# Optimization experiments

Hardware: AMD Instinct MI355X
Metric: run time of the kernel (lower is better)

The kernel has to match this reference:

```python
import jax, jax.numpy as jnp
import numpy as np

MASK_NUM = -2.0 ** 32 + 1.0  # additive mask value from the module


def setup_inputs() -> dict:
    key = jax.random.key(0)
    k1, k2, k3, k4 = jax.random.split(key, 4)
    BH, S, D = 32, 2048, 64   # batch*heads, seq, head_dim
    B = 2                      # true batch for key padding masks
    q = jax.random.normal(k1, (BH, S, D), dtype=jnp.float32)
    k = jax.random.normal(k2, (BH, S, D), dtype=jnp.float32)
    v = jax.random.normal(k3, (BH, S, D), dtype=jnp.float32)
    masks = jax.random.randint(k4, (B, S), 0, 2, dtype=jnp.int32)  # 1 = masked key
    return {"q": q, "k": k, "v": v, "masks": masks}


def reference(q, k, v, masks):
    # scores: [BH, Sq, Sk]
    d = q.shape[-1]
    scores = jnp.einsum("bqd,bkd->bqk", q, k) / jnp.sqrt(jnp.float32(d))
    # tile key-padding masks over heads: [B,Sk] -> [BH,Sk], add big negative
    tile = q.shape[0] // masks.shape[0]
    m = jnp.tile(masks.astype(jnp.float32), (tile, 1))  # [BH, Sk]
    scores = scores + m[:, None, :] * MASK_NUM
    attn = jax.nn.softmax(scores, axis=-1)
    # dropout rate is 0.0 -> identity
    out = jnp.einsum("bqk,bkd->bqd", attn, v)
    return out
```

## Files before the change

kernel.cpp:

```cpp
#include <hip/hip_runtime.h>
#include <hip/hip_bf16.h>


#define SQ 2048
#define DD 64
#define NT 32

typedef __attribute__((ext_vector_type(8)))  short bf16x8;
typedef __attribute__((ext_vector_type(16))) float f32x16;

#define LOG2E  1.4426950408889634f
#define QSCALE (0.125f * LOG2E)
#define MASKV  (-4294967295.0f * LOG2E)
#define THRL   (8.0f * LOG2E)

__device__ __forceinline__ short f2bf(float x) {
    union { float f; unsigned u; } a; a.f = x;
    unsigned r = a.u + 0x7fffu + ((a.u >> 16) & 1u);
    return (short)(r >> 16);
}
__device__ __forceinline__ int cvt_pk(float lo, float hi) {
    int r;
    asm("v_cvt_pk_bf16_f32 %0, %1, %2" : "=v"(r) : "v"(lo), "v"(hi));
    return r;
}
__device__ __forceinline__ int swz(int row, int colByte) {
    return row * 128 + (colByte ^ ((row & 7) << 4));
}

__global__ __launch_bounds__(256, 2) void attn_fwd(
    const float* __restrict__ q, const float* __restrict__ k,
    const float* __restrict__ v, const int* __restrict__ masks,
    float* __restrict__ out)
{
    __shared__ alignas(16) char smem[24576];
    char*  Kb = smem;
    char*  Vb = smem + 8192;
    float* Mf = (float*)(smem + 16384);

    const int x    = blockIdx.x;
    const int orig = (x & 7) * 64 + (x >> 3);
    const int h    = orig >> 4;
    const int qb   = orig & 15;
    const int tid  = threadIdx.x;
    const int w    = tid >> 6;
    const int lane = tid & 63;
    const int l31  = lane & 31;
    const int hi   = lane >> 5;

    const float* __restrict__ qh = q + (size_t)h * SQ * DD;
    const float* __restrict__ kh = k + (size_t)h * SQ * DD;
    const float* __restrict__ vh = v + (size_t)h * SQ * DD;
    const int*   __restrict__ mrow = masks + (h & 1) * SQ;

    {
        int4 a = *(const int4*)(mrow + tid * 8);
        int4 b = *(const int4*)(mrow + tid * 8 + 4);
        float4 fa = { a.x ? MASKV : 0.f, a.y ? MASKV : 0.f,
                      a.z ? MASKV : 0.f, a.w ? MASKV : 0.f };
        float4 fb = { b.x ? MASKV : 0.f, b.y ? MASKV : 0.f,
                      b.z ? MASKV : 0.f, b.w ? MASKV : 0.f };
        *(float4*)(Mf + tid * 8)     = fa;
        *(float4*)(Mf + tid * 8 + 4) = fb;
    }

    const int qrow = qb * 128 + w * 32 + l31;
    bf16x8 qf[4];
#pragma unroll
    for (int dc = 0; dc < 4; ++dc) {
        const float* p = qh + (size_t)qrow * DD + dc * 16 + hi * 8;
        float4 a = *(const float4*)p;
        float4 b = *(const float4*)(p + 4);
        bf16x8 f;
        f[0] = f2bf(a.x * QSCALE); f[1] = f2bf(a.y * QSCALE);
        f[2] = f2bf(a.z * QSCALE); f[3] = f2bf(a.w * QSCALE);
        f[4] = f2bf(b.x * QSCALE); f[5] = f2bf(b.y * QSCALE);
        f[6] = f2bf(b.z * QSCALE); f[7] = f2bf(b.w * QSCALE);
        qf[dc] = f;
    }

    f32x16 o[2];
#pragma unroll
    for (int dt = 0; dt < 2; ++dt)
#pragma unroll
      for (int i = 0; i < 16; ++i) o[dt][i] = 0.f;
    float m = -3.0e38f, l = 0.f;

    const int rK = tid >> 3, cK = tid & 7;
    const int kV = tid & 63, dV = (tid >> 6) * 8;

    float4 kA0, kA1, kB0, kB1, vA0, vA1, vB0, vB1;
#define LOADKV(kt)                                                        \
    {   const float* kpA = kh + (size_t)((kt) + rK)      * DD + 8 * cK;  \
        const float* kpB = kh + (size_t)((kt) + rK + 32) * DD + 8 * cK;  \
        const float* vpA = vh + (size_t)((kt) + kV) * DD + dV;           \
        const float* vpB = vpA + 32;                                      \
        kA0 = *(const float4*)kpA; kA1 = *(const float4*)(kpA + 4);      \
        kB0 = *(const float4*)kpB; kB1 = *(const float4*)(kpB + 4);      \
        vA0 = *(const float4*)vpA; vA1 = *(const float4*)(vpA + 4);      \
        vB0 = *(const float4*)vpB; vB1 = *(const float4*)(vpB + 4);      }

#define WRITEKV()                                                         \
    {   bf16x8 kw;                                                        \
        kw[0]=f2bf(kA0.x); kw[1]=f2bf(kA0.y); kw[2]=f2bf(kA0.z); kw[3]=f2bf(kA0.w); \
        kw[4]=f2bf(kA1.x); kw[5]=f2bf(kA1.y); kw[6]=f2bf(kA1.z); kw[7]=f2bf(kA1.w); \
        *(bf16x8*)(Kb + swz(rK, 16 * cK)) = kw;                           \
        kw[0]=f2bf(kB0.x); kw[1]=f2bf(kB0.y); kw[2]=f2bf(kB0.z); kw[3]=f2bf(kB0.w); \
        kw[4]=f2bf(kB1.x); kw[5]=f2bf(kB1.y); kw[6]=f2bf(kB1.z); kw[7]=f2bf(kB1.w); \
        *(bf16x8*)(Kb + swz(rK + 32, 16 * cK)) = kw;                      \
        float va[8] = {vA0.x, vA0.y, vA0.z, vA0.w, vA1.x, vA1.y, vA1.z, vA1.w}; \
        float vb[8] = {vB0.x, vB0.y, vB0.z, vB0.w, vB1.x, vB1.y, vB1.z, vB1.w}; \
        _Pragma("unroll")                                                 \
        for (int j = 0; j < 8; ++j) {                                     \
            *(short*)(Vb + (dV + j)      * 128 + ((2 * kV) ^ (j << 4))) = f2bf(va[j]); \
            *(short*)(Vb + (dV + 32 + j) * 128 + ((2 * kV) ^ (j << 4))) = f2bf(vb[j]); \
        }                                                                 }

    LOADKV(0)
    WRITEKV()
    __syncthreads();

    for (int it = 0; it < NT; ++it) {
        const int kt = it * 64;
        if (it + 1 < NT) LOADKV(kt + 64)

        const float* mf = Mf + kt;
        f32x16 s0, s1;
#pragma unroll
        for (int g = 0; g < 4; ++g) {
            float4 m0 = *(const float4*)(mf + 8 * g + 4 * hi);
            float4 m1 = *(const float4*)(mf + 32 + 8 * g + 4 * hi);
            s0[4*g+0] = m0.x; s0[4*g+1] = m0.y; s0[4*g+2] = m0.z; s0[4*g+3] = m0.w;
            s1[4*g+0] = m1.x; s1[4*g+1] = m1.y; s1[4*g+2] = m1.z; s1[4*g+3] = m1.w;
        }
#pragma unroll
        for (int dc = 0; dc < 4; ++dc) {
            bf16x8 k0 = *(const bf16x8*)(Kb + swz(l31,      32 * dc + 16 * hi));
            bf16x8 k1 = *(const bf16x8*)(Kb + swz(32 + l31, 32 * dc + 16 * hi));
            s0 = __builtin_amdgcn_mfma_f32_32x32x16_bf16(k0, qf[dc], s0, 0, 0, 0);
            s1 = __builtin_amdgcn_mfma_f32_32x32x16_bf16(k1, qf[dc], s1, 0, 0, 0);
        }

        float t[16];
#pragma unroll
        for (int i = 0; i < 16; ++i) t[i] = fmaxf(s0[i], s1[i]);
#pragma unroll
        for (int stp = 8; stp >= 1; stp >>= 1)
#pragma unroll
            for (int i = 0; i < stp; ++i) t[i] = fmaxf(t[i], t[i + stp]);
        float pmax = fmaxf(t[0], __shfl_xor(t[0], 32));

        float mn = m;
        if (!__all(pmax <= m + THRL)) {
            mn = fmaxf(m, pmax);
            float al = __builtin_amdgcn_exp2f(m - mn);
            l *= al;
#pragma unroll
            for (int dt = 0; dt < 2; ++dt)
#pragma unroll
              for (int i = 0; i < 16; ++i) o[dt][i] *= al;
            m = mn;
        }

        float p0[16], p1[16];
        float ps0 = 0.f, ps1 = 0.f;
#pragma unroll
        for (int i = 0; i < 16; ++i) {
            p0[i] = __builtin_amdgcn_exp2f(s0[i] - mn); ps0 += p0[i];
            p1[i] = __builtin_amdgcn_exp2f(s1[i] - mn); ps1 += p1[i];
        }
        float ps = ps0 + ps1;
        l += ps + __shfl_xor(ps, 32);

        int pk[2][4][2], sw[2][4][2];
#pragma unroll
        for (int g = 0; g < 4; ++g) {
            pk[0][g][0] = cvt_pk(p0[4*g+0], p0[4*g+1]);
            pk[0][g][1] = cvt_pk(p0[4*g+2], p0[4*g+3]);
            pk[1][g][0] = cvt_pk(p1[4*g+0], p1[4*g+1]);
            pk[1][g][1] = cvt_pk(p1[4*g+2], p1[4*g+3]);
        }
#pragma unroll
        for (int kb = 0; kb < 2; ++kb)
#pragma unroll
          for (int g = 0; g < 4; ++g)
#pragma unroll
            for (int j = 0; j < 2; ++j)
                sw[kb][g][j] = __shfl_xor(pk[kb][g][j], 32);

#pragma unroll
        for (int kc = 0; kc < 4; ++kc) {
            const int kb = kc >> 1, kp = kc & 1;
            union { int u[4]; bf16x8 b; } pu;
            pu.u[0] = hi ? sw[kb][2*kp+1][0] : pk[kb][2*kp][0];
            pu.u[1] = hi ? sw[kb][2*kp+1][1] : pk[kb][2*kp][1];
            pu.u[2] = hi ? pk[kb][2*kp+1][0] : sw[kb][2*kp][0];
            pu.u[3] = hi ? pk[kb][2*kp+1][1] : sw[kb][2*kp][1];
#pragma unroll
            for (int dt = 0; dt < 2; ++dt) {
                bf16x8 vf = *(const bf16x8*)(Vb + swz(32 * dt + l31, 32 * kc + 16 * hi));
                o[dt] = __builtin_amdgcn_mfma_f32_32x32x16_bf16(vf, pu.b, o[dt], 0, 0, 0);
            }
        }

        __syncthreads();
        if (it + 1 < NT) WRITEKV()
        __syncthreads();
    }

    const float invl = 1.0f / l;
    float* op = out + (size_t)h * SQ * DD + (size_t)qrow * DD;
#pragma unroll
    for (int dt = 0; dt < 2; ++dt)
#pragma unroll
      for (int g = 0; g < 4; ++g) {
        float4 r = { o[dt][4*g+0] * invl, o[dt][4*g+1] * invl,
                     o[dt][4*g+2] * invl, o[dt][4*g+3] * invl };
        *(float4*)(op + 32 * dt + 8 * g + 4 * hi) = r;
      }
}

extern "C" void kernel_launch(void* const* d_in, const int* in_sizes, int n_in,
                              void* d_out, int out_size, void* d_ws, size_t ws_size,
                              hipStream_t stream) {
    const float* q = (const float*)d_in[0];
    const float* k = (const float*)d_in[1];
    const float* v = (const float*)d_in[2];
    const int* masks = (const int*)d_in[3];
    float* out = (float*)d_out;
    attn_fwd<<<dim3(512), dim3(256), 0, stream>>>(q, k, v, masks, out);
}
```

Measured before the change: 76.03 us.

## Double-buffer K/V in LDS and use permlane32 swaps with hardware bf16 conversion

```diff
diff --git a/kernel.cpp b/kernel.cpp
--- a/kernel.cpp
+++ b/kernel.cpp
@@ -8,17 +8,13 @@
 
 typedef __attribute__((ext_vector_type(8)))  short bf16x8;
 typedef __attribute__((ext_vector_type(16))) float f32x16;
+typedef __attribute__((ext_vector_type(2)))  unsigned uint2v;
 
 #define LOG2E  1.4426950408889634f
 #define QSCALE (0.125f * LOG2E)
 #define MASKV  (-4294967295.0f * LOG2E)
 #define THRL   (8.0f * LOG2E)
 
-__device__ __forceinline__ short f2bf(float x) {
-    union { float f; unsigned u; } a; a.f = x;
-    unsigned r = a.u + 0x7fffu + ((a.u >> 16) & 1u);
-    return (short)(r >> 16);
-}
 __device__ __forceinline__ int cvt_pk(float lo, float hi) {
     int r;
     asm("v_cvt_pk_bf16_f32 %0, %1, %2" : "=v"(r) : "v"(lo), "v"(hi));
@@ -26,6 +22,38 @@
 }
 __device__ __forceinline__ int swz(int row, int colByte) {
     return row * 128 + (colByte ^ ((row & 7) << 4));
+}
+__device__ __forceinline__ float xmax(float x) {
+#if __has_builtin(__builtin_amdgcn_permlane32_swap)
+    union { float f; unsigned u; } a; a.f = x;
+    uint2v r = __builtin_amdgcn_permlane32_swap(a.u, a.u, false, false);
+    union { unsigned u; float f; } p0, p1; p0.u = r[0]; p1.u = r[1];
+    return fmaxf(p0.f, p1.f);
+#else
+    return fmaxf(x, __shfl_xor(x, 32));
+#endif
+}
+__device__ __forceinline__ float xsum(float x) {
+#if __has_builtin(__builtin_amdgcn_permlane32_swap)
+    union { float f; unsigned u; } a; a.f = x;
+    uint2v r = __builtin_amdgcn_permlane32_swap(a.u, a.u, false, false);
+    union { unsigned u; float f; } p0, p1; p0.u = r[0]; p1.u = r[1];
+    return p0.f + p1.f;
+#else
+    return x + __shfl_xor(x, 32);
+#endif
+}
+__device__ __forceinline__ void plswap2(unsigned a, unsigned b,
+                                        unsigned& lo01, unsigned& hi23, int hi) {
+#if __has_builtin(__builtin_amdgcn_permlane32_swap)
+    uint2v r = __builtin_amdgcn_permlane32_swap(a, b, false, false);
+    lo01 = r[0]; hi23 = r[1];
+#else
+    unsigned pa = (unsigned)__shfl_xor((int)a, 32);
+    unsigned pb = (unsigned)__shfl_xor((int)b, 32);
+    lo01 = hi ? pb : a;
+    hi23 = hi ? b : pa;
+#endif
 }
 
 __global__ __launch_bounds__(256, 2) void attn_fwd(
@@ -33,10 +61,8 @@
     const float* __restrict__ v, const int* __restrict__ masks,
     float* __restrict__ out)
 {
-    __shared__ alignas(16) char smem[24576];
-    char*  Kb = smem;
-    char*  Vb = smem + 8192;
-    float* Mf = (float*)(smem + 16384);
+    __shared__ alignas(16) char smem[40960];
+    float* Mf = (float*)(smem + 32768);
 
     const int x    = blockIdx.x;
     const int orig = (x & 7) * 64 + (x >> 3);
@@ -71,12 +97,12 @@
         const float* p = qh + (size_t)qrow * DD + dc * 16 + hi * 8;
         float4 a = *(const float4*)p;
         float4 b = *(const float4*)(p + 4);
-        bf16x8 f;
-        f[0] = f2bf(a.x * QSCALE); f[1] = f2bf(a.y * QSCALE);
-        f[2] = f2bf(a.z * QSCALE); f[3] = f2bf(a.w * QSCALE);
-        f[4] = f2bf(b.x * QSCALE); f[5] = f2bf(b.y * QSCALE);
-        f[6] = f2bf(b.z * QSCALE); f[7] = f2bf(b.w * QSCALE);
-        qf[dc] = f;
+        union { int i[4]; bf16x8 v; } f;
+        f.i[0] = cvt_pk(a.x * QSCALE, a.y * QSCALE);
+        f.i[1] = cvt_pk(a.z * QSCALE, a.w * QSCALE);
+        f.i[2] = cvt_pk(b.x * QSCALE, b.y * QSCALE);
+        f.i[3] = cvt_pk(b.z * QSCALE, b.w * QSCALE);
+        qf[dc] = f.v;
     }
 
     f32x16 o[2];
@@ -87,42 +113,45 @@
     float m = -3.0e38f, l = 0.f;
 
     const int rK = tid >> 3, cK = tid & 7;
-    const int kV = tid & 63, dV = (tid >> 6) * 8;
+    const int aV = tid & 31, dV = (tid >> 5) * 8;
 
     float4 kA0, kA1, kB0, kB1, vA0, vA1, vB0, vB1;
 #define LOADKV(kt)                                                        \
-    {   const float* kpA = kh + (size_t)((kt) + rK)      * DD + 8 * cK;  \
-        const float* kpB = kh + (size_t)((kt) + rK + 32) * DD + 8 * cK;  \
-        const float* vpA = vh + (size_t)((kt) + kV) * DD + dV;           \
-        const float* vpB = vpA + 32;                                      \
+    {   const float* kpA = kh + (size_t)((kt) + rK) * DD + 8 * cK;       \
+        const float* kpB = kpA + 32 * DD;                                 \
+        const float* vpA = vh + (size_t)((kt) + 2 * aV) * DD + dV;       \
+        const float* vpB = vpA + DD;                                      \
         kA0 = *(const float4*)kpA; kA1 = *(const float4*)(kpA + 4);      \
         kB0 = *(const float4*)kpB; kB1 = *(const float4*)(kpB + 4);      \
         vA0 = *(const float4*)vpA; vA1 = *(const float4*)(vpA + 4);      \
         vB0 = *(const float4*)vpB; vB1 = *(const float4*)(vpB + 4);      }
 
-#define WRITEKV()                                                         \
-    {   bf16x8 kw;                                                        \
-        kw[0]=f2bf(kA0.x); kw[1]=f2bf(kA0.y); kw[2]=f2bf(kA0.z); kw[3]=f2bf(kA0.w); \
-        kw[4]=f2bf(kA1.x); kw[5]=f2bf(kA1.y); kw[6]=f2bf(kA1.z); kw[7]=f2bf(kA1.w); \
-        *(bf16x8*)(Kb + swz(rK, 16 * cK)) = kw;                           \
-        kw[0]=f2bf(kB0.x); kw[1]=f2bf(kB0.y); kw[2]=f2bf(kB0.z); kw[3]=f2bf(kB0.w); \
-        kw[4]=f2bf(kB1.x); kw[5]=f2bf(kB1.y); kw[6]=f2bf(kB1.z); kw[7]=f2bf(kB1.w); \
-        *(bf16x8*)(Kb + swz(rK + 32, 16 * cK)) = kw;                      \
+#define WRITEKV(Kp, Vp)                                                   \
+    {   union { int i[4]; bf16x8 b; } kw;                                 \
+        kw.i[0] = cvt_pk(kA0.x, kA0.y); kw.i[1] = cvt_pk(kA0.z, kA0.w);  \
+        kw.i[2] = cvt_pk(kA1.x, kA1.y); kw.i[3] = cvt_pk(kA1.z, kA1.w);  \
+        *(bf16x8*)((Kp) + swz(rK, 16 * cK)) = kw.b;                       \
+        kw.i[0] = cvt_pk(kB0.x, kB0.y); kw.i[1] = cvt_pk(kB0.z, kB0.w);  \
+        kw.i[2] = cvt_pk(kB1.x, kB1.y); kw.i[3] = cvt_pk(kB1.z, kB1.w);  \
+        *(bf16x8*)((Kp) + swz(rK + 32, 16 * cK)) = kw.b;                  \
         float va[8] = {vA0.x, vA0.y, vA0.z, vA0.w, vA1.x, vA1.y, vA1.z, vA1.w}; \
         float vb[8] = {vB0.x, vB0.y, vB0.z, vB0.w, vB1.x, vB1.y, vB1.z, vB1.w}; \
         _Pragma("unroll")                                                 \
-        for (int j = 0; j < 8; ++j) {                                     \
-            *(short*)(Vb + (dV + j)      * 128 + ((2 * kV) ^ (j << 4))) = f2bf(va[j]); \
-            *(short*)(Vb + (dV + 32 + j) * 128 + ((2 * kV) ^ (j << 4))) = f2bf(vb[j]); \
-        }                                                                 }
+        for (int j = 0; j < 8; ++j)                                       \
+            *(unsigned*)((Vp) + (dV + j) * 128 + ((4 * aV) ^ (j << 4)))  \
+                = (unsigned)cvt_pk(va[j], vb[j]);                         }
 
     LOADKV(0)
-    WRITEKV()
+    WRITEKV(smem, smem + 8192)
     __syncthreads();
 
+    int boff = 0;
     for (int it = 0; it < NT; ++it) {
         const int kt = it * 64;
-        if (it + 1 < NT) LOADKV(kt + 64)
+        const bool more = (it + 1 < NT);
+        if (more) LOADKV(kt + 64)
+        char* Kb = smem + boff;
+        char* Vb = Kb + 8192;
 
         const float* mf = Mf + kt;
         f32x16 s0, s1;
@@ -133,6 +162,7 @@
             s0[4*g+0] = m0.x; s0[4*g+1] = m0.y; s0[4*g+2] = m0.z; s0[4*g+3] = m0.w;
             s1[4*g+0] = m1.x; s1[4*g+1] = m1.y; s1[4*g+2] = m1.z; s1[4*g+3] = m1.w;
         }
+        __builtin_amdgcn_s_setprio(1);
 #pragma unroll
         for (int dc = 0; dc < 4; ++dc) {
             bf16x8 k0 = *(const bf16x8*)(Kb + swz(l31,      32 * dc + 16 * hi));
@@ -140,6 +170,7 @@
             s0 = __builtin_amdgcn_mfma_f32_32x32x16_bf16(k0, qf[dc], s0, 0, 0, 0);
             s1 = __builtin_amdgcn_mfma_f32_32x32x16_bf16(k1, qf[dc], s1, 0, 0, 0);
         }
+        __builtin_amdgcn_s_setprio(0);
 
         float t[16];
 #pragma unroll
@@ -148,7 +179,7 @@
         for (int stp = 8; stp >= 1; stp >>= 1)
 #pragma unroll
             for (int i = 0; i < stp; ++i) t[i] = fmaxf(t[i], t[i + stp]);
-        float pmax = fmaxf(t[0], __shfl_xor(t[0], 32));
+        float pmax = xmax(t[0]);
 
         float mn = m;
         if (!__all(pmax <= m + THRL)) {
@@ -163,49 +194,53 @@
         }
 
         float p0[16], p1[16];
-        float ps0 = 0.f, ps1 = 0.f;
 #pragma unroll
         for (int i = 0; i < 16; ++i) {
-            p0[i] = __builtin_amdgcn_exp2f(s0[i] - mn); ps0 += p0[i];
-            p1[i] = __builtin_amdgcn_exp2f(s1[i] - mn); ps1 += p1[i];
-        }
-        float ps = ps0 + ps1;
-        l += ps + __shfl_xor(ps, 32);
-
-        int pk[2][4][2], sw[2][4][2];
+            p0[i] = __builtin_amdgcn_exp2f(s0[i] - mn);
+            p1[i] = __builtin_amdgcn_exp2f(s1[i] - mn);
+        }
+        float u[16];
+#pragma unroll
+        for (int i = 0; i < 16; ++i) u[i] = p0[i] + p1[i];
+#pragma unroll
+        for (int stp = 8; stp >= 1; stp >>= 1)
+#pragma unroll
+            for (int i = 0; i < stp; ++i) u[i] += u[i + stp];
+        l += xsum(u[0]);
+
+        unsigned pk[2][4][2];
 #pragma unroll
         for (int g = 0; g < 4; ++g) {
-            pk[0][g][0] = cvt_pk(p0[4*g+0], p0[4*g+1]);
-            pk[0][g][1] = cvt_pk(p0[4*g+2], p0[4*g+3]);
-            pk[1][g][0] = cvt_pk(p1[4*g+0], p1[4*g+1]);
-            pk[1][g][1] = cvt_pk(p1[4*g+2], p1[4*g+3]);
-        }
-#pragma unroll
-        for (int kb = 0; kb < 2; ++kb)
-#pragma unroll
-          for (int g = 0; g < 4; ++g)
-#pragma unroll
-            for (int j = 0; j < 2; ++j)
-                sw[kb][g][j] = __shfl_xor(pk[kb][g][j], 32);
-
+            pk[0][g][0] = (unsigned)cvt_pk(p0[4*g+0], p0[4*g+1]);
+            pk[0][g][1] = (unsigned)cvt_pk(p0[4*g+2], p0[4*g+3]);
+            pk[1][g][0] = (unsigned)cvt_pk(p1[4*g+0], p1[4*g+1]);
+            pk[1][g][1] = (unsigned)cvt_pk(p1[4*g+2], p1[4*g+3]);
+        }
+
+        if (more) {
+            char* Kn = smem + (boff ^ 16384);
+            WRITEKV(Kn, Kn + 8192)
+        }
+
+        __builtin_amdgcn_s_setprio(1);
 #pragma unroll
         for (int kc = 0; kc < 4; ++kc) {
             const int kb = kc >> 1, kp = kc & 1;
-            union { int u[4]; bf16x8 b; } pu;
-            pu.u[0] = hi ? sw[kb][2*kp+1][0] : pk[kb][2*kp][0];
-            pu.u[1] = hi ? sw[kb][2*kp+1][1] : pk[kb][2*kp][1];
-            pu.u[2] = hi ? pk[kb][2*kp+1][0] : sw[kb][2*kp][0];
-            pu.u[3] = hi ? pk[kb][2*kp+1][1] : sw[kb][2*kp][1];
+            union { unsigned u[4]; bf16x8 b; } pu;
+            unsigned lo0, hi0, lo1, hi1;
+            plswap2(pk[kb][2*kp][0], pk[kb][2*kp+1][0], lo0, hi0, hi);
+            plswap2(pk[kb][2*kp][1], pk[kb][2*kp+1][1], lo1, hi1, hi);
+            pu.u[0] = lo0; pu.u[1] = lo1; pu.u[2] = hi0; pu.u[3] = hi1;
 #pragma unroll
             for (int dt = 0; dt < 2; ++dt) {
                 bf16x8 vf = *(const bf16x8*)(Vb + swz(32 * dt + l31, 32 * kc + 16 * hi));
                 o[dt] = __builtin_amdgcn_mfma_f32_32x32x16_bf16(vf, pu.b, o[dt], 0, 0, 0);
             }
         }
+        __builtin_amdgcn_s_setprio(0);
 
         __syncthreads();
-        if (it + 1 < NT) WRITEKV()
-        __syncthreads();
+        boff ^= 16384;
     }
 
     const float invl = 1.0f / l;
```

After: 62.65 us. -17.6%, faster.
